# Kernel tuning notes

Hardware: AMD Instinct MI355X
Metric: run time of the kernel (lower is better)

## Reference

```python
import jax, jax.numpy as jnp
import numpy as np

B, N, H, NH, M = 4, 8192, 1024, 16, 64
D = H // NH  # head_dim = 64
SCALE = D ** -0.5


def setup_inputs() -> dict:
    key = jax.random.key(0)
    ks = jax.random.split(key, 10)
    inp = {
        'x': jax.random.normal(ks[0], (B, N, H), jnp.float32),
        'c': jax.random.normal(ks[1], (B, H), jnp.float32),
        'w_kv': jax.random.normal(ks[2], (H, 2 * H), jnp.float32) * (H ** -0.5),
        'b_kv': jnp.zeros((2 * H,), jnp.float32),
        'w_temp': jax.random.normal(ks[3], (H, NH), jnp.float32) * (H ** -0.5),
        'b_temp': jnp.zeros((NH,), jnp.float32),
        'xq': jax.random.normal(ks[4], (NH, M, D), jnp.float32) * (D ** -0.5),
        'qkv_proj': jax.random.normal(ks[5], (NH, D, 3 * D), jnp.float32) * 0.02,
        'w_out': jax.random.normal(ks[6], (H, H), jnp.float32) * (H ** -0.5),
        'b_out': jnp.zeros((H,), jnp.float32),
    }
    return inp


def reference(x, c, w_kv, b_kv, w_temp, b_temp, xq, qkv_proj, w_out, b_out):
    b, n, h = x.shape
    # kv slice projections -> [b, h, n, d]
    kv = x @ w_kv + b_kv
    xk, xv = jnp.split(kv, 2, axis=-1)
    xk = xk.reshape(b, n, NH, D).transpose(0, 2, 1, 3)
    xv = xv.reshape(b, n, NH, D).transpose(0, 2, 1, 3)
    # per-token learned temperature: [b, n, heads] -> [b, heads, 1, n]
    temperature = 0.5 + jax.nn.softplus(x @ w_temp + b_temp)
    temperature = temperature.transpose(0, 2, 1)[:, :, None, :]
    # slice scores and softmax over SLICE (query) dim m
    slice_scores = jnp.einsum('hmd,bhnd->bhmn', xq, xk)
    slice_weights = jax.nn.softmax(slice_scores / temperature, axis=-2)
    slice_norm = slice_weights.sum(axis=-1)  # [b, h, m]
    slice_token = jnp.einsum('bhmn,bhnd->bhmd', slice_weights, xv)
    slice_token = slice_token / (slice_norm[..., None] + 1e-5)
    # tiny intra-slice 'attention' (faithfully elementwise, softmax over d)
    qkv = jnp.einsum('bhmd,hde->bhme', slice_token, qkv_proj)
    q_t, k_t, v_t = jnp.split(qkv, 3, axis=-1)
    dots = q_t * k_t * SCALE          # einsum 'bhqd,bhdq->bhqd' == elementwise
    attn = jax.nn.softmax(dots, axis=-1)
    out_slice_token = attn * v_t       # einsum 'bhqd,bhqd->bhqd' == elementwise
    # scatter back to tokens via slice_weights
    out_x = jnp.einsum('bhmd,bhmn->bhnd', out_slice_token, slice_weights)
    out_x = out_x.transpose(0, 2, 1, 3).reshape(b, n, h)
    return out_x @ w_out + b_out
```

## Files before the change

### kernel.cpp

```cpp
#include <hip/hip_runtime.h>
#include <hip/hip_bf16.h>


#define NTOK 32768
#define HH   1024
#define NHD  16
#define DD   64

typedef short short8 __attribute__((ext_vector_type(8)));
typedef float f32x4 __attribute__((ext_vector_type(4)));

#define AS1 __attribute__((address_space(1)))
#define AS3 __attribute__((address_space(3)))

__device__ __forceinline__ void glds16(const void* g, void* l) {
  __builtin_amdgcn_global_load_lds((const AS1 void*)g, (AS3 void*)l, 16, 0, 0);
}

__device__ __forceinline__ void split1(float v, __hip_bfloat16& h, __hip_bfloat16& l) {
  h = __float2bfloat16(v);
  l = __float2bfloat16(v - __bfloat162float(h));
}


__global__ __launch_bounds__(256) void k_acat_t(const float* __restrict__ w_kv,
                                                const float* __restrict__ xq,
                                                __hip_bfloat16* __restrict__ wbth,
                                                __hip_bfloat16* __restrict__ wbtl) {
  int hd = blockIdx.x >> 3, kt = blockIdx.x & 7, k0 = kt * 128;
  __shared__ float xqs[64 * 65];
  __shared__ float wks[128 * 65];
  int t = threadIdx.x;
  for (int j = 0; j < 16; ++j) {
    int idx = t + 256 * j; int m = idx >> 6, d = idx & 63;
    xqs[m * 65 + d] = xq[hd * 4096 + idx];
  }
  for (int j = 0; j < 32; ++j) {
    int idx = t + 256 * j; int r = idx >> 6, c = idx & 63;
    wks[r * 65 + c] = w_kv[(size_t)(k0 + r) * 2048 + hd * 64 + c];
  }
  __syncthreads();
  int m = t & 63, kg = t >> 6;
  __hip_bfloat16 hbuf[32], lbuf[32];
  for (int i = 0; i < 32; ++i) {
    int k = kg * 32 + i;
    float s = 0.f;
    #pragma unroll 8
    for (int d = 0; d < 64; ++d) s = fmaf(wks[k * 65 + d], xqs[m * 65 + d], s);
    split1(s, hbuf[i], lbuf[i]);
  }
  size_t o = (size_t)(hd * 64 + m) * 1024 + k0 + kg * 32;
  for (int i = 0; i < 32; i += 8) {
    *(uint4*)&wbth[o + i] = *(uint4*)&hbuf[i];
    *(uint4*)&wbtl[o + i] = *(uint4*)&lbuf[i];
  }
}

__global__ __launch_bounds__(256) void k_tsplit(const float* __restrict__ src, int ld,
                                                __hip_bfloat16* __restrict__ dh,
                                                __hip_bfloat16* __restrict__ dl) {
  __shared__ float tile[64 * 65];
  int br = blockIdx.y * 64, bc = blockIdx.x * 64;
  int t = threadIdx.x;
  for (int j = 0; j < 16; ++j) {
    int idx = t + 256 * j; int r = idx >> 6, c = idx & 63;
    tile[r * 65 + c] = src[(size_t)(br + r) * ld + bc + c];
  }
  __syncthreads();
  for (int j = 0; j < 16; ++j) {
    int idx = t + 256 * j; int c = idx >> 6, r = idx & 63;
    float v = tile[r * 65 + c];
    __hip_bfloat16 hv, lv; split1(v, hv, lv);
    size_t o = (size_t)(bc + c) * 1024 + br + r;
    dh[o] = hv; dl[o] = lv;
  }
}

__global__ void k_split(const float* __restrict__ src, __hip_bfloat16* __restrict__ hi,
                        __hip_bfloat16* __restrict__ lo) {
  size_t base = ((size_t)blockIdx.x * 256 + threadIdx.x) * 8;
  float4 v0 = *(const float4*)&src[base];
  float4 v1 = *(const float4*)&src[base + 4];
  float vv[8] = {v0.x, v0.y, v0.z, v0.w, v1.x, v1.y, v1.z, v1.w};
  __hip_bfloat16 h8[8], l8[8];
  #pragma unroll
  for (int i = 0; i < 8; ++i) split1(vv[i], h8[i], l8[i]);
  *(uint4*)&hi[base] = *(uint4*)h8;
  *(uint4*)&lo[base] = *(uint4*)l8;
}

__global__ __launch_bounds__(512, 2) void k_mfma8(
    const __hip_bfloat16* __restrict__ Ah, const __hip_bfloat16* __restrict__ Al,
    const __hip_bfloat16* __restrict__ Bh, const __hip_bfloat16* __restrict__ Bl,
    const float* __restrict__ bias, float* __restrict__ C, int ldc) {
  __shared__ __align__(16) char lds[131072];
  const int t = threadIdx.x;
  const int w = t >> 6, lane = t & 63;

  const int gx = gridDim.x;
  const int nwg = gx * gridDim.y;
  const int bid = blockIdx.y * gx + blockIdx.x;
  const int swzb = (bid & 7) * (nwg >> 3) + (bid >> 3);
  const int n0 = (swzb % gx) * 256;
  const int m0 = (swzb / gx) * 256;

  const int wr = w >> 2, wc = w & 3;
  const int fm = lane & 15, kq = lane >> 4;

  int offA[8], offB[4];
  #pragma unroll
  for (int i = 0; i < 8; ++i) {
    int row = wr * 128 + i * 16 + fm;
    offA[i] = (row >> 1) * 128 + ((((row & 1) << 2) | kq) ^ ((row >> 1) & 7)) * 16;
  }
  #pragma unroll
  for (int j = 0; j < 4; ++j) {
    int row = wc * 64 + j * 16 + fm;
    offB[j] = (row >> 1) * 128 + ((((row & 1) << 2) | kq) ^ ((row >> 1) & 7)) * 16;
  }

  const int sp = lane >> 3, su = (lane & 7) ^ sp;
  const int srow = 2 * sp + (su >> 2);
  const int scol = (su & 3) * 8;
  const int aO0 = (m0 + w * 16 + srow) * 1024 + scol;
  const int aO1 = aO0 + 128 * 1024;
  const int bO0 = (n0 + w * 16 + srow) * 1024 + scol;
  const int bO1 = bO0 + 128 * 1024;
  const int ldst = w * 1024 + lane * 16;

  f32x4 acc[8][4];
  #pragma unroll
  for (int i = 0; i < 8; ++i)
    #pragma unroll
    for (int j = 0; j < 4; ++j) acc[i][j] = (f32x4){0.f, 0.f, 0.f, 0.f};

  auto stage = [&](int ts, char* buf) {
    int koff = ts * 32;
    glds16(Ah + aO0 + koff, buf + ldst);
    glds16(Ah + aO1 + koff, buf + 8192 + ldst);
    glds16(Al + aO0 + koff, buf + 16384 + ldst);
    glds16(Al + aO1 + koff, buf + 24576 + ldst);
    glds16(Bh + bO0 + koff, buf + 32768 + ldst);
    glds16(Bh + bO1 + koff, buf + 40960 + ldst);
    glds16(Bl + bO0 + koff, buf + 49152 + ldst);
    glds16(Bl + bO1 + koff, buf + 57344 + ldst);
  };

  stage(0, lds);
  asm volatile("s_waitcnt vmcnt(0)" ::: "memory");
  __builtin_amdgcn_s_barrier();
  __builtin_amdgcn_sched_barrier(0);

  #pragma unroll 2
  for (int tt = 0; tt < 32; ++tt) {
    char* rb = &lds[(tt & 1) * 65536];
    char* wb = &lds[((tt + 1) & 1) * 65536];

    short8 ah[8], bh[4], xb[4];
    #pragma unroll
    for (int i = 0; i < 8; ++i) ah[i] = *(const short8*)(rb + offA[i]);
    #pragma unroll
    for (int j = 0; j < 4; ++j) bh[j] = *(const short8*)(rb + 32768 + offB[j]);
    if (tt < 31) stage(tt + 1, wb);
    __builtin_amdgcn_s_barrier();
    __builtin_amdgcn_sched_barrier(0);
    __builtin_amdgcn_s_setprio(1);
    #pragma unroll
    for (int i = 0; i < 8; ++i)
      #pragma unroll
      for (int j = 0; j < 4; ++j)
        acc[i][j] = __builtin_amdgcn_mfma_f32_16x16x32_bf16(ah[i], bh[j], acc[i][j], 0, 0, 0);
    __builtin_amdgcn_s_setprio(0);
    __builtin_amdgcn_s_barrier();
    __builtin_amdgcn_sched_barrier(0);

    #pragma unroll
    for (int j = 0; j < 4; ++j) xb[j] = *(const short8*)(rb + 49152 + offB[j]);
    __builtin_amdgcn_s_barrier();
    __builtin_amdgcn_sched_barrier(0);
    __builtin_amdgcn_s_setprio(1);
    #pragma unroll
    for (int i = 0; i < 8; ++i)
      #pragma unroll
      for (int j = 0; j < 4; ++j)
        acc[i][j] = __builtin_amdgcn_mfma_f32_16x16x32_bf16(ah[i], xb[j], acc[i][j], 0, 0, 0);
    __builtin_amdgcn_s_setprio(0);
    __builtin_amdgcn_s_barrier();
    __builtin_amdgcn_sched_barrier(0);

    #pragma unroll
    for (int i = 0; i < 8; ++i) ah[i] = *(const short8*)(rb + 16384 + offA[i]);
    __builtin_amdgcn_s_barrier();
    __builtin_amdgcn_sched_barrier(0);
    __builtin_amdgcn_s_setprio(1);
    #pragma unroll
    for (int i = 0; i < 8; ++i)
      #pragma unroll
      for (int j = 0; j < 4; ++j)
        acc[i][j] = __builtin_amdgcn_mfma_f32_16x16x32_bf16(ah[i], bh[j], acc[i][j], 0, 0, 0);
    __builtin_amdgcn_s_setprio(0);
    asm volatile("s_waitcnt vmcnt(0)" ::: "memory");
    __builtin_amdgcn_s_barrier();
    __builtin_amdgcn_sched_barrier(0);
  }

  asm volatile("s_waitcnt vmcnt(0)" ::: "memory");

  const int cm = (lane >> 4) * 4, cn = lane & 15;
  #pragma unroll
  for (int j = 0; j < 4; ++j) {
    int col = n0 + wc * 64 + j * 16 + cn;
    float bbv = bias[col];
    #pragma unroll
    for (int i = 0; i < 8; ++i) {
      int row = m0 + wr * 128 + i * 16 + cm;
      f32x4 v = acc[i][j];
      #pragma unroll
      for (int r = 0; r < 4; ++r)
        C[(size_t)(row + r) * ldc + col] = v[r] + bbv;
    }
  }
}

__global__ __launch_bounds__(256) void k_acat(const float* __restrict__ w_kv,
                                              const float* __restrict__ xq,
                                              float* __restrict__ wbig) {
  int h = blockIdx.x >> 3, kt = blockIdx.x & 7, k0 = kt * 128;
  __shared__ float xqs[64 * 68];
  __shared__ float wks[128 * 68];
  int t = threadIdx.x;
  for (int j = 0; j < 16; ++j) {
    int idx = t + 256 * j; int m = idx >> 6, d = idx & 63;
    xqs[m * 68 + d] = xq[h * 4096 + idx];
  }
  for (int j = 0; j < 32; ++j) {
    int idx = t + 256 * j; int r = idx >> 6, c = idx & 63;
    wks[r * 68 + c] = w_kv[(k0 + r) * 2048 + h * 64 + c];
  }
  __syncthreads();
  int k = t >> 1, half = t & 1;
  float out[32];
  for (int mi = 0; mi < 32; ++mi) {
    int m = half * 32 + mi;
    float s = 0.f;
    #pragma unroll 8
    for (int d = 0; d < 64; ++d) s = fmaf(wks[k * 68 + d], xqs[m * 68 + d], s);
    out[mi] = s;
  }
  float* dst = &wbig[(k0 + k) * 2048 + h * 64 + half * 32];
  for (int mi = 0; mi < 32; mi += 4)
    *(float4*)(dst + mi) = make_float4(out[mi], out[mi + 1], out[mi + 2], out[mi + 3]);
}

__global__ void k_copyv(const float* __restrict__ w_kv, float* __restrict__ wbig) {
  int idx4 = blockIdx.x * 256 + threadIdx.x;
  int k = idx4 >> 8, j4 = idx4 & 255;
  int off = k * 2048 + 1024 + j4 * 4;
  *(float4*)(wbig + off) = *(const float4*)(w_kv + off);
}

__global__ void k_bias1(const float* __restrict__ xq, const float* __restrict__ b_kv,
                        float* __restrict__ bias1) {
  int j = blockIdx.x * 256 + threadIdx.x;
  if (j < 1024) {
    int h = j >> 6, m = j & 63;
    float s = 0.f;
    for (int d = 0; d < 64; ++d) s = fmaf(xq[h * 4096 + m * 64 + d], b_kv[h * 64 + d], s);
    bias1[j] = s;
  } else {
    bias1[j] = b_kv[j];
  }
}

__global__ __launch_bounds__(256) void k_temp(const float* __restrict__ x,
                                              const float* __restrict__ w_temp,
                                              const float* __restrict__ b_temp,
                                              float* __restrict__ T) {
  __shared__ float xs[16 * 1028];
  int t = threadIdx.x;
  int bn0 = blockIdx.x * 16;
  for (int j = 0; j < 16; ++j) {
    int idx4 = t + 256 * j; int row = idx4 >> 8, c4 = (idx4 & 255) * 4;
    *(float4*)&xs[row * 1028 + c4] = *(const float4*)&x[(bn0 + row) * 1024 + c4];
  }
  __syncthreads();
  int tok = t >> 4, j = t & 15;
  float z = b_temp[j];
  for (int k = 0; k < 1024; ++k) z = fmaf(xs[tok * 1028 + k], w_temp[k * 16 + j], z);
  float sp = fmaxf(z, 0.f) + log1pf(expf(-fabsf(z)));
  T[(bn0 + tok) * 16 + j] = 0.5f + sp;
}

__global__ __launch_bounds__(256) void k_gemm(const float* __restrict__ A, int lda,
                                              const float* __restrict__ Bm, int ldb,
                                              const float* __restrict__ bias,
                                              float* __restrict__ C, int ldc, int K) {
  __shared__ float As[8 * 132];
  __shared__ float Bs[8 * 132];
  int t = threadIdx.x;
  int m0 = blockIdx.y * 128, n0 = blockIdx.x * 128;
  int ar = t >> 1, ac = (t & 1) * 4;
  int bk = t >> 5, bc = (t & 31) * 4;
  const float* Ag = A + (size_t)(m0 + ar) * lda + ac;
  const float* Bg = Bm + (size_t)bk * ldb + n0 + bc;
  int tx = t & 15, ty = t >> 4;
  float acc[8][8] = {};
  float4 a4 = *(const float4*)Ag;
  float4 b4 = *(const float4*)Bg;
  for (int kt = 0; kt < K; kt += 8) {
    __syncthreads();
    As[(ac + 0) * 132 + ar] = a4.x;
    As[(ac + 1) * 132 + ar] = a4.y;
    As[(ac + 2) * 132 + ar] = a4.z;
    As[(ac + 3) * 132 + ar] = a4.w;
    *(float4*)&Bs[bk * 132 + bc] = b4;
    __syncthreads();
    if (kt + 8 < K) {
      a4 = *(const float4*)(Ag + kt + 8);
      b4 = *(const float4*)(Bg + (size_t)(kt + 8) * ldb);
    }
    #pragma unroll
    for (int k = 0; k < 8; ++k) {
      float av[8], bv[8];
      *(float4*)&av[0] = *(float4*)&As[k * 132 + ty * 8];
      *(float4*)&av[4] = *(float4*)&As[k * 132 + ty * 8 + 4];
      *(float4*)&bv[0] = *(float4*)&Bs[k * 132 + tx * 4];
      *(float4*)&bv[4] = *(float4*)&Bs[k * 132 + 64 + tx * 4];
      #pragma unroll
      for (int i = 0; i < 8; ++i)
        #pragma unroll
        for (int j = 0; j < 8; ++j) acc[i][j] = fmaf(av[i], bv[j], acc[i][j]);
    }
  }
  float4 bb0 = *(const float4*)&bias[n0 + tx * 4];
  float4 bb1 = *(const float4*)&bias[n0 + 64 + tx * 4];
  #pragma unroll
  for (int i = 0; i < 8; ++i) {
    float* crow = C + (size_t)(m0 + ty * 8 + i) * ldc + n0;
    float4 o0 = make_float4(acc[i][0] + bb0.x, acc[i][1] + bb0.y,
                            acc[i][2] + bb0.z, acc[i][3] + bb0.w);
    float4 o1 = make_float4(acc[i][4] + bb1.x, acc[i][5] + bb1.y,
                            acc[i][6] + bb1.z, acc[i][7] + bb1.w);
    *(float4*)&crow[tx * 4] = o0;
    *(float4*)&crow[64 + tx * 4] = o1;
  }
}

__global__ __launch_bounds__(256) void k_smax(float* __restrict__ S, const float* __restrict__ T,
                                              float* __restrict__ token, float* __restrict__ norm) {
  int pair = blockIdx.x >> 3, chunk = blockIdx.x & 7;
  int b = pair >> 4, h = pair & 15;
  __shared__ float sm[128 * 68];
  __shared__ float xv[128 * 68];
  int t = threadIdx.x;
  int m = t >> 2, dg = t & 3;
  float acc[16] = {};
  float nacc = 0.f;
  for (int s = 0; s < 8; ++s) {
    int bn0 = b * 8192 + chunk * 1024 + s * 128;
    for (int jj = 0; jj < 8; ++jj) {
      int idx4 = t + 256 * jj; int row = idx4 >> 4, c4 = (idx4 & 15) * 4;
      int g = (bn0 + row) * 2048 + h * 64 + c4;
      *(float4*)&sm[row * 68 + c4] = *(const float4*)&S[g];
      *(float4*)&xv[row * 68 + c4] = *(const float4*)&S[g + 1024];
    }
    __syncthreads();
    if (t < 128) {
      float tt = T[(bn0 + t) * 16 + h];
      float inv = 1.f / tt;
      float* row = &sm[t * 68];
      float mx = -1e30f;
      for (int mm = 0; mm < 64; ++mm) mx = fmaxf(mx, row[mm]);
      float sum = 0.f;
      for (int mm = 0; mm < 64; ++mm) { float e = expf((row[mm] - mx) * inv); row[mm] = e; sum += e; }
      float sinv = 1.f / sum;
      for (int mm = 0; mm < 64; ++mm) row[mm] *= sinv;
    }
    __syncthreads();
    for (int jj = 0; jj < 8; ++jj) {
      int idx4 = t + 256 * jj; int row = idx4 >> 4, c4 = (idx4 & 15) * 4;
      int g = (bn0 + row) * 2048 + h * 64 + c4;
      *(float4*)&S[g] = *(const float4*)&sm[row * 68 + c4];
    }
    for (int n = 0; n < 128; ++n) {
      float w = sm[n * 68 + m];
      if (dg == 0) nacc += w;
      const float* xr = &xv[n * 68 + dg * 16];
      #pragma unroll
      for (int q = 0; q < 4; ++q) {
        float4 v = *(const float4*)&xr[q * 4];
        acc[q * 4 + 0] = fmaf(w, v.x, acc[q * 4 + 0]);
        acc[q * 4 + 1] = fmaf(w, v.y, acc[q * 4 + 1]);
        acc[q * 4 + 2] = fmaf(w, v.z, acc[q * 4 + 2]);
        acc[q * 4 + 3] = fmaf(w, v.w, acc[q * 4 + 3]);
      }
    }
    __syncthreads();
  }
  int tb = pair * 4096 + m * 64 + dg * 16;
  for (int q = 0; q < 16; ++q) atomicAdd(&token[tb + q], acc[q]);
  if (dg == 0) atomicAdd(&norm[pair * 64 + m], nacc);
}

__global__ __launch_bounds__(256) void k_stagec(const float* __restrict__ token,
                                                const float* __restrict__ norm,
                                                const float* __restrict__ proj,
                                                float* __restrict__ ost) {
  int pair = blockIdx.x; int h = pair & 15;
  __shared__ float st[64 * 68];
  __shared__ float qk[64 * 196];
  int t = threadIdx.x;
  for (int j = 0; j < 16; ++j) {
    int idx = t + 256 * j; int m = idx >> 6, d = idx & 63;
    st[m * 68 + d] = token[pair * 4096 + idx] / (norm[pair * 64 + m] + 1e-5f);
  }
  __syncthreads();
  for (int idx = t; idx < 64 * 192; idx += 256) {
    int m = idx / 192, e = idx % 192;
    float s = 0.f;
    const float* pr = &proj[h * 12288 + e];
    const float* sr = &st[m * 68];
    for (int d = 0; d < 64; ++d) s = fmaf(sr[d], pr[d * 192], s);
    qk[m * 196 + e] = s;
  }
  __syncthreads();
  if (t < 64) {
    const float* q = &qk[t * 196];
    float dots[64];
    float mx = -1e30f;
    for (int d = 0; d < 64; ++d) { dots[d] = q[d] * q[64 + d] * 0.125f; mx = fmaxf(mx, dots[d]); }
    float sum = 0.f;
    for (int d = 0; d < 64; ++d) { dots[d] = expf(dots[d] - mx); sum += dots[d]; }
    float sinv = 1.f / sum;
    for (int d = 0; d < 64; ++d) ost[pair * 4096 + t * 64 + d] = dots[d] * sinv * q[128 + d];
  }
}

__global__ __launch_bounds__(256) void k_staged(float* __restrict__ S, const float* __restrict__ ost) {
  int pair = blockIdx.x >> 6, chunk = blockIdx.x & 63;
  int b = pair >> 4, h = pair & 15;
  __shared__ float ws[128 * 68];
  int t = threadIdx.x;
  int bn0 = b * 8192 + chunk * 128;
  for (int jj = 0; jj < 8; ++jj) {
    int idx4 = t + 256 * jj; int row = idx4 >> 4, c4 = (idx4 & 15) * 4;
    *(float4*)&ws[row * 68 + c4] = *(const float4*)&S[(bn0 + row) * 2048 + h * 64 + c4];
  }
  int d = t & 63, ng = t >> 6;
  float o[64];
  #pragma unroll
  for (int mm = 0; mm < 64; ++mm) o[mm] = ost[pair * 4096 + mm * 64 + d];
  __syncthreads();
  for (int i = 0; i < 32; ++i) {
    int n = ng + 4 * i;
    const float* wr = &ws[n * 68];
    float s = 0.f;
    #pragma unroll
    for (int mm = 0; mm < 64; ++mm) s = fmaf(wr[mm], o[mm], s);
    S[(bn0 + n) * 2048 + 1024 + h * 64 + d] = s;
  }
}

__global__ __launch_bounds__(256) void k_staged_bf(const float* __restrict__ S,
                                                   const float* __restrict__ ost,
                                                   __hip_bfloat16* __restrict__ oxh,
                                                   __hip_bfloat16* __restrict__ oxl) {
  int pair = blockIdx.x >> 6, chunk = blockIdx.x & 63;
  int b = pair >> 4, hd = pair & 15;
  __shared__ float ws[128 * 68];
  int t = threadIdx.x;
  int bn0 = b * 8192 + chunk * 128;
  for (int jj = 0; jj < 8; ++jj) {
    int idx4 = t + 256 * jj; int row = idx4 >> 4, c4 = (idx4 & 15) * 4;
    *(float4*)&ws[row * 68 + c4] = *(const float4*)&S[(bn0 + row) * 2048 + hd * 64 + c4];
  }
  int d = t & 63, ng = t >> 6;
  float o[64];
  #pragma unroll
  for (int mm = 0; mm < 64; ++mm) o[mm] = ost[pair * 4096 + mm * 64 + d];
  __syncthreads();
  for (int i = 0; i < 32; ++i) {
    int n = ng + 4 * i;
    const float* wr = &ws[n * 68];
    float s = 0.f;
    #pragma unroll
    for (int mm = 0; mm < 64; ++mm) s = fmaf(wr[mm], o[mm], s);
    __hip_bfloat16 hv, lv; split1(s, hv, lv);
    size_t oo = (size_t)(bn0 + n) * 1024 + hd * 64 + d;
    oxh[oo] = hv; oxl[oo] = lv;
  }
}

extern "C" void kernel_launch(void* const* d_in, const int* in_sizes, int n_in,
                              void* d_out, int out_size, void* d_ws, size_t ws_size,
                              hipStream_t stream) {
  const float* x      = (const float*)d_in[0];
  const float* w_kv   = (const float*)d_in[2];
  const float* b_kv   = (const float*)d_in[3];
  const float* w_temp = (const float*)d_in[4];
  const float* b_temp = (const float*)d_in[5];
  const float* xq     = (const float*)d_in[6];
  const float* proj   = (const float*)d_in[7];
  const float* w_out  = (const float*)d_in[8];
  const float* b_out  = (const float*)d_in[9];
  float* out = (float*)d_out;

  float* ws    = (float*)d_ws;
  float* S     = ws;
  float* T     = S + 67108864;
  float* BIAS1 = T + 524288;
  float* TOKEN = BIAS1 + 2048;
  float* NORM  = TOKEN + 262144;
  float* OST   = NORM + 4096;
  float* FEND  = OST + 262144;
  __hip_bfloat16* WbTh = (__hip_bfloat16*)FEND;
  __hip_bfloat16* WbTl = WbTh + 2097152;
  __hip_bfloat16* WoTh = WbTl + 2097152;
  __hip_bfloat16* WoTl = WoTh + 1048576;
  __hip_bfloat16* XH   = WoTl + 1048576;
  __hip_bfloat16* XL   = XH + 33554432;
  const size_t need_fast = 419454976ULL;

  hipMemsetAsync(TOKEN, 0, (262144 + 4096) * sizeof(float), stream);
  k_bias1<<<8, 256, 0, stream>>>(xq, b_kv, BIAS1);
  k_temp<<<2048, 256, 0, stream>>>(x, w_temp, b_temp, T);

  if (ws_size >= need_fast) {
    k_acat_t<<<128, 256, 0, stream>>>(w_kv, xq, WbTh, WbTl);
    k_tsplit<<<dim3(16, 16), 256, 0, stream>>>(w_kv + 1024, 2048,
                                               WbTh + 1048576, WbTl + 1048576);
    k_tsplit<<<dim3(16, 16), 256, 0, stream>>>(w_out, 1024, WoTh, WoTl);
    k_split<<<16384, 256, 0, stream>>>(x, XH, XL);
    k_mfma8<<<dim3(8, 128), 512, 0, stream>>>(XH, XL, WbTh, WbTl, BIAS1, S, 2048);
    k_smax<<<512, 256, 0, stream>>>(S, T, TOKEN, NORM);
    k_stagec<<<64, 256, 0, stream>>>(TOKEN, NORM, proj, OST);
    k_staged_bf<<<4096, 256, 0, stream>>>(S, OST, XH, XL);
    k_mfma8<<<dim3(4, 128), 512, 0, stream>>>(XH, XL, WoTh, WoTl, b_out, out, 1024);
  } else {
    float* WBIG = (float*)WbTh;
    k_acat<<<128, 256, 0, stream>>>(w_kv, xq, WBIG);
    k_copyv<<<1024, 256, 0, stream>>>(w_kv, WBIG);
    k_gemm<<<dim3(16, 256), 256, 0, stream>>>(x, 1024, WBIG, 2048, BIAS1, S, 2048, 1024);
    k_smax<<<512, 256, 0, stream>>>(S, T, TOKEN, NORM);
    k_stagec<<<64, 256, 0, stream>>>(TOKEN, NORM, proj, OST);
    k_staged<<<4096, 256, 0, stream>>>(S, OST);
    k_gemm<<<dim3(8, 256), 256, 0, stream>>>(S + 1024, 2048, w_out, 1024, b_out, out, 1024, 1024);
  }
}
```

Measured before the change: 1.534 ms.

## Split hi/lo operand stages into a four-buffer, three-ahead async LDS pipeline

```diff
diff --git a/kernel.cpp b/kernel.cpp
--- a/kernel.cpp
+++ b/kernel.cpp
@@ -134,36 +134,34 @@
     #pragma unroll
     for (int j = 0; j < 4; ++j) acc[i][j] = (f32x4){0.f, 0.f, 0.f, 0.f};
 
-  auto stage = [&](int ts, char* buf) {
-    int koff = ts * 32;
-    glds16(Ah + aO0 + koff, buf + ldst);
-    glds16(Ah + aO1 + koff, buf + 8192 + ldst);
-    glds16(Al + aO0 + koff, buf + 16384 + ldst);
-    glds16(Al + aO1 + koff, buf + 24576 + ldst);
-    glds16(Bh + bO0 + koff, buf + 32768 + ldst);
-    glds16(Bh + bO1 + koff, buf + 40960 + ldst);
-    glds16(Bl + bO0 + koff, buf + 49152 + ldst);
-    glds16(Bl + bO1 + koff, buf + 57344 + ldst);
+  auto stage = [&](int ts) {
+    int koff = (ts >> 1) * 32;
+    char* buf = &lds[(ts & 3) * 32768];
+    const __hip_bfloat16* As = (ts & 1) ? Al : Ah;
+    const __hip_bfloat16* Bs = (ts & 1) ? Bl : Bh;
+    glds16(As + aO0 + koff, buf + ldst);
+    glds16(As + aO1 + koff, buf + 8192 + ldst);
+    glds16(Bs + bO0 + koff, buf + 16384 + ldst);
+    glds16(Bs + bO1 + koff, buf + 24576 + ldst);
   };
 
-  stage(0, lds);
-  asm volatile("s_waitcnt vmcnt(0)" ::: "memory");
+  stage(0); stage(1); stage(2);
+  asm volatile("s_waitcnt vmcnt(8)" ::: "memory");
   __builtin_amdgcn_s_barrier();
   __builtin_amdgcn_sched_barrier(0);
 
-  #pragma unroll 2
-  for (int tt = 0; tt < 32; ++tt) {
-    char* rb = &lds[(tt & 1) * 65536];
-    char* wb = &lds[((tt + 1) & 1) * 65536];
-
-    short8 ah[8], bh[4], xb[4];
-    #pragma unroll
-    for (int i = 0; i < 8; ++i) ah[i] = *(const short8*)(rb + offA[i]);
-    #pragma unroll
-    for (int j = 0; j < 4; ++j) bh[j] = *(const short8*)(rb + 32768 + offB[j]);
-    if (tt < 31) stage(tt + 1, wb);
-    __builtin_amdgcn_s_barrier();
-    __builtin_amdgcn_sched_barrier(0);
+  short8 ah[8], bh[4], xb[4];
+  for (int k = 0; k < 32; ++k) {
+    const int v0 = 2 * k, v1 = v0 + 1;
+    const char* rb0 = &lds[(v0 & 3) * 32768];
+    const char* rb1 = &lds[(v1 & 3) * 32768];
+
+    int ts0 = v0 + 3; if (ts0 > 63) ts0 = 63;
+    stage(ts0);
+    #pragma unroll
+    for (int i = 0; i < 8; ++i) ah[i] = *(const short8*)(rb0 + offA[i]);
+    #pragma unroll
+    for (int j = 0; j < 4; ++j) bh[j] = *(const short8*)(rb0 + 16384 + offB[j]);
     __builtin_amdgcn_s_setprio(1);
     #pragma unroll
     for (int i = 0; i < 8; ++i)
@@ -171,13 +169,14 @@
       for (int j = 0; j < 4; ++j)
         acc[i][j] = __builtin_amdgcn_mfma_f32_16x16x32_bf16(ah[i], bh[j], acc[i][j], 0, 0, 0);
     __builtin_amdgcn_s_setprio(0);
+    asm volatile("s_waitcnt vmcnt(8)" ::: "memory");
     __builtin_amdgcn_s_barrier();
     __builtin_amdgcn_sched_barrier(0);
 
-    #pragma unroll
-    for (int j = 0; j < 4; ++j) xb[j] = *(const short8*)(rb + 49152 + offB[j]);
-    __builtin_amdgcn_s_barrier();
-    __builtin_amdgcn_sched_barrier(0);
+    int ts1 = v1 + 3; if (ts1 > 63) ts1 = 63;
+    stage(ts1);
+    #pragma unroll
+    for (int j = 0; j < 4; ++j) xb[j] = *(const short8*)(rb1 + 16384 + offB[j]);
     __builtin_amdgcn_s_setprio(1);
     #pragma unroll
     for (int i = 0; i < 8; ++i)
@@ -185,13 +184,8 @@
       for (int j = 0; j < 4; ++j)
         acc[i][j] = __builtin_amdgcn_mfma_f32_16x16x32_bf16(ah[i], xb[j], acc[i][j], 0, 0, 0);
     __builtin_amdgcn_s_setprio(0);
-    __builtin_amdgcn_s_barrier();
-    __builtin_amdgcn_sched_barrier(0);
-
-    #pragma unroll
-    for (int i = 0; i < 8; ++i) ah[i] = *(const short8*)(rb + 16384 + offA[i]);
-    __builtin_amdgcn_s_barrier();
-    __builtin_amdgcn_sched_barrier(0);
+    #pragma unroll
+    for (int i = 0; i < 8; ++i) ah[i] = *(const short8*)(rb1 + offA[i]);
     __builtin_amdgcn_s_setprio(1);
     #pragma unroll
     for (int i = 0; i < 8; ++i)
@@ -199,12 +193,13 @@
       for (int j = 0; j < 4; ++j)
         acc[i][j] = __builtin_amdgcn_mfma_f32_16x16x32_bf16(ah[i], bh[j], acc[i][j], 0, 0, 0);
     __builtin_amdgcn_s_setprio(0);
-    asm volatile("s_waitcnt vmcnt(0)" ::: "memory");
+    asm volatile("s_waitcnt vmcnt(8)" ::: "memory");
     __builtin_amdgcn_s_barrier();
     __builtin_amdgcn_sched_barrier(0);
   }
 
   asm volatile("s_waitcnt vmcnt(0)" ::: "memory");
+  __builtin_amdgcn_sched_barrier(0);
 
   const int cm = (lane >> 4) * 4, cn = lane & 15;
   #pragma unroll
```

Measured after the change: 1.417 ms. 7.7% less time.
